# Optimization experiments

Measured on AMD Instinct MI355X. Metric: run time of the kernel, lower is better.

Reference implementation:

```python
import jax, jax.numpy as jnp
import numpy as np

BN_EPS = 1e-5
LN_EPS = 1e-5

N_NODES = 50000
N_EDGES = 800000
D_IN = 128
D_HID = 512


def _batchnorm(h, gamma, beta):
    # training-mode BatchNorm1d: biased variance over the node/batch dim
    m = jnp.mean(h, axis=0)
    v = jnp.mean(jnp.square(h - m), axis=0)
    return (h - m) * jax.lax.rsqrt(v + BN_EPS) * gamma + beta


def setup_inputs() -> dict:
    key = jax.random.key(0)
    ks = jax.random.split(key, 8)
    x = jax.random.normal(ks[0], (N_NODES, D_IN), dtype=jnp.float32)
    edge_index = jax.random.randint(ks[1], (2, N_EDGES), 0, N_NODES, dtype=jnp.int64)
    s1 = 1.0 / np.sqrt(D_IN)
    s2 = 1.0 / np.sqrt(D_HID)
    W1 = jax.random.uniform(ks[2], (D_IN, D_HID), jnp.float32, -s1, s1)
    b1 = jax.random.uniform(ks[3], (D_HID,), jnp.float32, -s1, s1)
    W2 = jax.random.uniform(ks[4], (D_HID, D_IN), jnp.float32, -s2, s2)
    b2 = jax.random.uniform(ks[5], (D_IN,), jnp.float32, -s2, s2)
    return {
        "x": x,
        "edge_index": edge_index,
        "W1": W1, "b1": b1,
        "bn1_g": jnp.ones((D_HID,), jnp.float32), "bn1_b": jnp.zeros((D_HID,), jnp.float32),
        "W2": W2, "b2": b2,
        "bn2_g": jnp.ones((D_IN,), jnp.float32), "bn2_b": jnp.zeros((D_IN,), jnp.float32),
        "ln_g": jnp.ones((D_IN,), jnp.float32), "ln_b": jnp.zeros((D_IN,), jnp.float32),
    }


def reference(x, edge_index, W1, b1, bn1_g, bn1_b, W2, b2, bn2_g, bn2_b, ln_g, ln_b):
    n = x.shape[0]
    src = edge_index[0]
    dst = edge_index[1]
    # GIN aggregation: sum of neighbor (source) features at each destination node
    agg = jax.ops.segment_sum(x[src], dst, num_segments=n)  # [N, D_IN]
    h = x + agg  # (1 + eps) * x + agg, eps = 0
    # MLP: Linear -> BN -> ReLU -> Linear -> BN -> ReLU (final activation)
    h = jax.nn.relu(_batchnorm(h @ W1 + b1, bn1_g, bn1_b))  # [N, D_HID]
    h = jax.nn.relu(_batchnorm(h @ W2 + b2, bn2_g, bn2_b))  # [N, D_IN]
    # residual + LayerNorm (dropout p=0 -> identity)
    out = h + x
    m = jnp.mean(out, axis=-1, keepdims=True)
    v = jnp.mean(jnp.square(out - m), axis=-1, keepdims=True)
    out = (out - m) * jax.lax.rsqrt(v + LN_EPS) * ln_g + ln_b
    return out
```

## Files before the change

### kernel.cpp

```cpp
#include <hip/hip_runtime.h>
#include <stdint.h>

#define N_NODES 50000
#define N_EDGES 800000
#define D_IN    128
#define D_HID   512
#define NPAD    50048
#define NTILES  391
#define SCAN_NB 196
#define G_TILES 782
#define G_BLOCKS 128

typedef __attribute__((ext_vector_type(8))) short short8;
typedef __attribute__((ext_vector_type(4))) float f32x4;

__device__ __forceinline__ float bf2f(unsigned short u) {
    union { unsigned int i; float f; } v; v.i = ((unsigned int)u) << 16; return v.f;
}
__device__ __forceinline__ unsigned short f2bf(float f) {
    union { float f; unsigned int i; } v; v.f = f;
    unsigned int r = v.i + 0x7fffu + ((v.i >> 16) & 1u);
    return (unsigned short)(r >> 16);
}
__device__ __forceinline__ float loadP(const void* p, long i, int isf) {
    return isf ? ((const float*)p)[i] : bf2f(((const unsigned short*)p)[i]);
}

__global__ void k_init(const void* __restrict__ x, const int* __restrict__ ei,
                       float* __restrict__ stats, int* __restrict__ counts,
                       int* __restrict__ flags) {
    int t = threadIdx.x;
    if (blockIdx.x < 197) {
        int i = blockIdx.x * 256 + t;
        if (i < 384) stats[1024 + i] = 0.f;
        else if (i < 384 + N_NODES) counts[i - 384] = 0;
    } else {
        __shared__ int sh[2];
        if (t == 0) { sh[0] = 0; sh[1] = 1; }
        __syncthreads();
        const unsigned short* xu = (const unsigned short*)x;
        for (int i = t; i < 8192; i += 256)
            if (((xu[i] >> 7) & 0xFF) == 0xFF) sh[0] = 1;
        for (int k = t; k < 64; k += 256)
            if (ei[2 * k + 1] != 0) sh[1] = 0;
        __syncthreads();
        if (t == 0) { flags[0] = sh[0]; flags[1] = sh[1]; }
    }
}

__global__ void k_transpose2(const void* __restrict__ W1, const void* __restrict__ W2,
                             unsigned short* __restrict__ w1t, unsigned short* __restrict__ w2t,
                             const int* __restrict__ flags) {
    int isf = flags[0];
    int idx = blockIdx.x * 256 + threadIdx.x;
    if (idx < D_IN * D_HID) {
        int n = idx >> 7, k = idx & 127;
        int src = k * D_HID + n;
        w1t[idx] = isf ? f2bf(((const float*)W1)[src])
                       : ((const unsigned short*)W1)[src];
    } else {
        int j = idx - D_IN * D_HID;
        int n = j >> 9, k = j & 511;
        int src = k * D_IN + n;
        w2t[j] = isf ? f2bf(((const float*)W2)[src])
                     : ((const unsigned short*)W2)[src];
    }
}

__global__ void k_count(const int* __restrict__ ei, int* __restrict__ counts,
                        const int* __restrict__ flags) {
    int i64 = flags[1];
    int e = blockIdx.x * 256 + threadIdx.x;
    int d = i64 ? ei[2 * N_EDGES + 2 * e] : ei[N_EDGES + e];
    d = min(max(d, 0), N_NODES - 1);
    atomicAdd(&counts[d], 1);
}

__global__ __launch_bounds__(256) void k_scan_block(const int* __restrict__ counts,
                                                    int* __restrict__ rowptr,
                                                    int* __restrict__ partials) {
    __shared__ int a[256], b[256];
    int t = threadIdx.x;
    int idx = blockIdx.x * 256 + t;
    int c = (idx < N_NODES) ? counts[idx] : 0;
    a[t] = c;
    __syncthreads();
    int* src = a; int* dst = b;
    for (int off = 1; off < 256; off <<= 1) {
        dst[t] = src[t] + ((t >= off) ? src[t - off] : 0);
        __syncthreads();
        int* tmp = src; src = dst; dst = tmp;
    }
    if (idx < N_NODES) rowptr[idx] = src[t] - c;
    if (t == 255) partials[blockIdx.x] = src[255];
}

__global__ __launch_bounds__(256) void k_scan_part(int* __restrict__ partials) {
    __shared__ int a[256], b[256];
    int t = threadIdx.x;
    int c = (t < SCAN_NB) ? partials[t] : 0;
    a[t] = c;
    __syncthreads();
    int* src = a; int* dst = b;
    for (int off = 1; off < 256; off <<= 1) {
        dst[t] = src[t] + ((t >= off) ? src[t - off] : 0);
        __syncthreads();
        int* tmp = src; src = dst; dst = tmp;
    }
    if (t < SCAN_NB) partials[t] = src[t] - c;
}

__global__ void k_scan_add(int* __restrict__ rowptr, int* __restrict__ cursor,
                           const int* __restrict__ partials) {
    int idx = blockIdx.x * 256 + threadIdx.x;
    if (idx < N_NODES) {
        int v = rowptr[idx] + partials[blockIdx.x];
        rowptr[idx] = v;
        cursor[idx] = v;
    } else if (idx == N_NODES) {
        rowptr[N_NODES] = N_EDGES;
    }
}

__global__ void k_fill(const int* __restrict__ ei, int* __restrict__ cursor,
                       int* __restrict__ bucket, const int* __restrict__ flags) {
    int i64 = flags[1];
    int e = blockIdx.x * 256 + threadIdx.x;
    int s, d;
    if (i64) { s = ei[2 * e]; d = ei[2 * N_EDGES + 2 * e]; }
    else     { s = ei[e];     d = ei[N_EDGES + e]; }
    s = min(max(s, 0), N_NODES - 1);
    d = min(max(d, 0), N_NODES - 1);
    int pos = atomicAdd(&cursor[d], 1);
    bucket[pos] = s;
}

__global__ __launch_bounds__(256) void k_gather(const int* __restrict__ rowptr,
                                                const int* __restrict__ bucket,
                                                const void* __restrict__ x,
                                                unsigned short* __restrict__ agg,
                                                const int* __restrict__ flags) {
    int isf = flags[0];
    int w = threadIdx.x >> 6, lane = threadIdx.x & 63;
    int row = blockIdx.x * 4 + w;
    float a0 = 0.f, a1 = 0.f;
    if (row < N_NODES) {
        int beg = rowptr[row], end = rowptr[row + 1];
        if (isf) {
            const float* xf = (const float*)x;
            float2 v = *(const float2*)(xf + (size_t)row * D_IN + lane * 2);
            a0 = v.x; a1 = v.y;
            int j = beg;
            for (; j + 4 <= end; j += 4) {
                int s0 = bucket[j], s1 = bucket[j + 1], s2 = bucket[j + 2], s3 = bucket[j + 3];
                float2 n0 = *(const float2*)(xf + (size_t)s0 * D_IN + lane * 2);
                float2 n1 = *(const float2*)(xf + (size_t)s1 * D_IN + lane * 2);
                float2 n2 = *(const float2*)(xf + (size_t)s2 * D_IN + lane * 2);
                float2 n3 = *(const float2*)(xf + (size_t)s3 * D_IN + lane * 2);
                a0 += (n0.x + n1.x) + (n2.x + n3.x);
                a1 += (n0.y + n1.y) + (n2.y + n3.y);
            }
            for (; j < end; j++) {
                float2 n = *(const float2*)(xf + (size_t)bucket[j] * D_IN + lane * 2);
                a0 += n.x; a1 += n.y;
            }
        } else {
            const unsigned int* xu = (const unsigned int*)x;
            unsigned int u = xu[(size_t)row * 64 + lane];
            a0 = bf2f(u & 0xffff); a1 = bf2f(u >> 16);
            int j = beg;
            for (; j + 4 <= end; j += 4) {
                int s0 = bucket[j], s1 = bucket[j + 1], s2 = bucket[j + 2], s3 = bucket[j + 3];
                unsigned int u0 = xu[(size_t)s0 * 64 + lane];
                unsigned int u1 = xu[(size_t)s1 * 64 + lane];
                unsigned int u2 = xu[(size_t)s2 * 64 + lane];
                unsigned int u3 = xu[(size_t)s3 * 64 + lane];
                a0 += (bf2f(u0 & 0xffff) + bf2f(u1 & 0xffff)) + (bf2f(u2 & 0xffff) + bf2f(u3 & 0xffff));
                a1 += (bf2f(u0 >> 16) + bf2f(u1 >> 16)) + (bf2f(u2 >> 16) + bf2f(u3 >> 16));
            }
            for (; j < end; j++) {
                unsigned int n = xu[(size_t)bucket[j] * 64 + lane];
                a0 += bf2f(n & 0xffff); a1 += bf2f(n >> 16);
            }
        }
    }
    unsigned int o = (unsigned int)f2bf(a0) | ((unsigned int)f2bf(a1) << 16);
    ((unsigned int*)agg)[(size_t)row * 64 + lane] = o;
}

__global__ __launch_bounds__(256) void k_gram(const unsigned short* __restrict__ aggb,
                                              float* __restrict__ Gpart,
                                              float* __restrict__ colsum) {
    __shared__ unsigned short ldsT[128 * 64];
    int t = threadIdx.x;
    int wid = t >> 6, lane = t & 63;
    int wm = wid & 1, wn = wid >> 1;
    int quad = lane >> 4, l16 = lane & 15;
    f32x4 acc[4][4] = {};
    float cs = 0.f;
    int cscol = t & 127, cskh = t >> 7;
    for (int tile = blockIdx.x; tile < G_TILES; tile += G_BLOCKS) {
        __syncthreads();
        size_t rowbase = (size_t)tile * 64;
#pragma unroll
        for (int jj = 0; jj < 2; jj++) {
            int j = t + jj * 256;
            int c = j >> 5, rp = j & 31;
            uint4 v0 = *(const uint4*)(aggb + (rowbase + 2 * rp) * 128 + c * 8);
            uint4 v1 = *(const uint4*)(aggb + (rowbase + 2 * rp + 1) * 128 + c * 8);
            const unsigned short* p0 = (const unsigned short*)&v0;
            const unsigned short* p1 = (const unsigned short*)&v1;
            int k = 2 * rp, kc = k >> 3, ko = k & 7;
#pragma unroll
            for (int e = 0; e < 8; e++) {
                int col = c * 8 + e;
                *(unsigned int*)(ldsT + col * 64 + ((kc ^ (col & 7)) * 8) + ko) =
                    (unsigned int)p0[e] | ((unsigned int)p1[e] << 16);
            }
        }
        __syncthreads();
#pragma unroll
        for (int ksub = 0; ksub < 2; ksub++) {
            short8 fa[4], fb[4];
#pragma unroll
            for (int mt = 0; mt < 4; mt++) {
                int col = wm * 64 + mt * 16 + l16;
                fa[mt] = *(const short8*)(ldsT + col * 64 + (((ksub * 4 + quad) ^ (col & 7)) * 8));
            }
#pragma unroll
            for (int nt = 0; nt < 4; nt++) {
                int col = wn * 64 + nt * 16 + l16;
                fb[nt] = *(const short8*)(ldsT + col * 64 + (((ksub * 4 + quad) ^ (col & 7)) * 8));
            }
#pragma unroll
            for (int mt = 0; mt < 4; mt++)
#pragma unroll
                for (int nt = 0; nt < 4; nt++)
                    acc[mt][nt] = __builtin_amdgcn_mfma_f32_16x16x32_bf16(fa[mt], fb[nt], acc[mt][nt], 0, 0, 0);
        }
#pragma unroll
        for (int kc = 0; kc < 4; kc++) {
            short8 v = *(const short8*)(ldsT + cscol * 64 + (((cskh * 4 + kc) ^ (cscol & 7)) * 8));
#pragma unroll
            for (int e = 0; e < 8; e++) cs += bf2f((unsigned short)v[e]);
        }
    }
    float* gp = Gpart + (size_t)blockIdx.x * 16384;
#pragma unroll
    for (int mt = 0; mt < 4; mt++)
#pragma unroll
        for (int nt = 0; nt < 4; nt++) {
            int m = wm * 64 + mt * 16 + quad * 4;
            int n = wn * 64 + nt * 16 + l16;
#pragma unroll
            for (int rg = 0; rg < 4; rg++)
                gp[(m + rg) * 128 + n] = acc[mt][nt][rg];
        }
    atomicAdd(&colsum[cscol], cs);
}

__global__ void k_gred(const float* __restrict__ Gpart, float* __restrict__ G) {
    int i = blockIdx.x * 256 + threadIdx.x;
    float s = 0.f;
#pragma unroll 8
    for (int b = 0; b < G_BLOCKS; b++) s += Gpart[(size_t)b * 16384 + i];
    G[i] = s;
}

__global__ __launch_bounds__(256) void k_bn1(const float* __restrict__ G,
                                             const float* __restrict__ colsum,
                                             const unsigned short* __restrict__ w1t,
                                             const void* __restrict__ b1,
                                             float* __restrict__ sum1,
                                             float* __restrict__ sumsq1,
                                             const int* __restrict__ flags) {
    int isf = flags[0];
    __shared__ float wsh[4][128];
    int t = threadIdx.x, wid = t >> 6, lane = t & 63;
    int n = blockIdx.x * 4 + wid;
    unsigned int u = *(const unsigned int*)(w1t + (size_t)n * 128 + lane * 2);
    wsh[wid][lane * 2] = bf2f(u & 0xffff);
    wsh[wid][lane * 2 + 1] = bf2f(u >> 16);
    __syncthreads();
    const float* w = wsh[wid];
    const f32x4* g0 = (const f32x4*)(G + (size_t)lane * 128);
    const f32x4* g1 = (const f32x4*)(G + (size_t)(lane + 64) * 128);
    float t0 = 0.f, t1 = 0.f;
#pragma unroll 4
    for (int q4 = 0; q4 < 32; q4++) {
        f32x4 a = g0[q4], b = g1[q4];
        float w0 = w[q4 * 4], w1 = w[q4 * 4 + 1], w2 = w[q4 * 4 + 2], w3 = w[q4 * 4 + 3];
        t0 += a[0] * w0 + a[1] * w1 + a[2] * w2 + a[3] * w3;
        t1 += b[0] * w0 + b[1] * w1 + b[2] * w2 + b[3] * w3;
    }
    float sq = w[lane] * t0 + w[lane + 64] * t1;
    float s  = w[lane] * colsum[lane] + w[lane + 64] * colsum[lane + 64];
#pragma unroll
    for (int m = 1; m < 64; m <<= 1) {
        sq += __shfl_xor(sq, m, 64);
        s  += __shfl_xor(s, m, 64);
    }
    if (lane == 0) {
        float b = loadP(b1, n, isf);
        sum1[n]   = s + (float)N_NODES * b;
        sumsq1[n] = sq + 2.f * b * s + (float)N_NODES * b * b;
    }
}

__global__ __launch_bounds__(256, 2) void k_mlp1(const unsigned short* __restrict__ aggc,
                                                 const unsigned short* __restrict__ w1t,
                                                 const void* __restrict__ b1,
                                                 const void* __restrict__ g1,
                                                 const void* __restrict__ bb1,
                                                 const float* __restrict__ sum1,
                                                 const float* __restrict__ sumsq1,
                                                 unsigned short* __restrict__ h1c,
                                                 const int* __restrict__ flags) {
    __shared__ unsigned short bufA[128 * 128];
    __shared__ unsigned short bufW[128 * 128];
    int isf = flags[0];
    int t = threadIdx.x;
    int m0 = (blockIdx.x >> 2) * 128;
    int nb = blockIdx.x & 3;
    int r = t >> 1, half = t & 1;
    int wid = t >> 6, lane = t & 63;
    int wm = wid & 1, wn = wid >> 1;
    int quad = lane >> 4, l16 = lane & 15;
#pragma unroll
    for (int i = 0; i < 8; i++) {
        int chunk = half * 8 + i;
        int sw = ((chunk ^ (r & 15)) * 8);
        *(uint4*)(bufA + r * 128 + sw) = *(const uint4*)(aggc + (size_t)(m0 + r) * 128 + chunk * 8);
        *(uint4*)(bufW + r * 128 + sw) = *(const uint4*)(w1t + (size_t)(nb * 128 + r) * 128 + chunk * 8);
    }
    __syncthreads();
    f32x4 acc[4][4] = {};
#pragma unroll
    for (int ks = 0; ks < 4; ks++) {
        short8 af[4], bw[4];
#pragma unroll
        for (int mt = 0; mt < 4; mt++)
            af[mt] = *(const short8*)(bufA + (wm * 64 + mt * 16 + l16) * 128 + (((ks * 4 + quad) ^ l16) * 8));
#pragma unroll
        for (int nt = 0; nt < 4; nt++)
            bw[nt] = *(const short8*)(bufW + (wn * 64 + nt * 16 + l16) * 128 + (((ks * 4 + quad) ^ l16) * 8));
#pragma unroll
        for (int mt = 0; mt < 4; mt++)
#pragma unroll
            for (int nt = 0; nt < 4; nt++)
                acc[mt][nt] = __builtin_amdgcn_mfma_f32_16x16x32_bf16(af[mt], bw[nt], acc[mt][nt], 0, 0, 0);
    }
    __syncthreads();
#pragma unroll
    for (int nt = 0; nt < 4; nt++) {
        int nl = wn * 64 + nt * 16 + l16;
        int n1 = nb * 128 + nl;
        float mz = sum1[n1] * (1.f / N_NODES);
        float vz = sumsq1[n1] * (1.f / N_NODES) - mz * mz;
        float inv = rsqrtf(fmaxf(vz, 0.f) + 1e-5f);
        float A = loadP(g1, n1, isf) * inv;
        float C = loadP(bb1, n1, isf) - mz * A + loadP(b1, n1, isf) * A;
        int ccw = nl >> 3, cl = nl & 7;
#pragma unroll
        for (int mt = 0; mt < 4; mt++)
#pragma unroll
            for (int rg = 0; rg < 4; rg++) {
                int R = wm * 64 + mt * 16 + quad * 4 + rg;
                bufA[R * 128 + ((ccw ^ (R & 15)) * 8) + cl] = f2bf(fmaxf(acc[mt][nt][rg] * A + C, 0.f));
            }
    }
    __syncthreads();
#pragma unroll
    for (int i = 0; i < 8; i++) {
        int idx = t + i * 256;
        int rr = idx >> 4, chunk = idx & 15;
        *(uint4*)(h1c + (size_t)(m0 + rr) * D_HID + nb * 128 + chunk * 8) =
            *(const uint4*)(bufA + rr * 128 + ((chunk ^ (rr & 15)) * 8));
    }
}

__global__ __launch_bounds__(256, 3) void k_mlp2(const unsigned short* __restrict__ h1c,
                                                 const unsigned short* __restrict__ w2t,
                                                 const void* __restrict__ b2,
                                                 unsigned short* __restrict__ h2c,
                                                 float* __restrict__ sum2,
                                                 float* __restrict__ sumsq2,
                                                 const int* __restrict__ flags,
                                                 int roff) {
    __shared__ unsigned short bufA[64 * 128];
    __shared__ unsigned short bufW[128 * 128];
    __shared__ float sred[256];
    int isf = flags[0];
    int t = threadIdx.x;
    int m0 = blockIdx.x * 64;
    int rw = t >> 1, halfw = t & 1;
    int wid = t >> 6, lane = t & 63;
    int wm = wid & 1, wn = wid >> 1;
    int quad = lane >> 4, l16 = lane & 15;
    sred[t] = 0.f;
    f32x4 acc[2][4] = {};
    for (int kb = 0; kb < 4; kb++) {
        __syncthreads();
#pragma unroll
        for (int i = 0; i < 4; i++) {
            int idx = t + i * 256;
            int rr = idx >> 4, chunk = idx & 15;
            *(uint4*)(bufA + rr * 128 + ((chunk ^ (rr & 15)) * 8)) =
                *(const uint4*)(h1c + (size_t)(m0 + rr) * D_HID + kb * 128 + chunk * 8);
        }
#pragma unroll
        for (int i = 0; i < 8; i++) {
            int chunk = halfw * 8 + i;
            *(uint4*)(bufW + rw * 128 + ((chunk ^ (rw & 15)) * 8)) =
                *(const uint4*)(w2t + (size_t)rw * D_HID + kb * 128 + chunk * 8);
        }
        __syncthreads();
#pragma unroll
        for (int ks = 0; ks < 4; ks++) {
            short8 af[2], bw[4];
#pragma unroll
            for (int mt = 0; mt < 2; mt++)
                af[mt] = *(const short8*)(bufA + (wm * 32 + mt * 16 + l16) * 128 + (((ks * 4 + quad) ^ l16) * 8));
#pragma unroll
            for (int nt = 0; nt < 4; nt++)
                bw[nt] = *(const short8*)(bufW + (wn * 64 + nt * 16 + l16) * 128 + (((ks * 4 + quad) ^ l16) * 8));
#pragma unroll
            for (int mt = 0; mt < 2; mt++)
#pragma unroll
                for (int nt = 0; nt < 4; nt++)
                    acc[mt][nt] = __builtin_amdgcn_mfma_f32_16x16x32_bf16(af[mt], bw[nt], acc[mt][nt], 0, 0, 0);
        }
    }
    __syncthreads();
#pragma unroll
    for (int nt = 0; nt < 4; nt++) {
        int n = wn * 64 + nt * 16 + l16;
        float bias = loadP(b2, n, isf);
        float s = 0.f, ss = 0.f;
#pragma unroll
        for (int mt = 0; mt < 2; mt++) {
            int Rl = wm * 32 + mt * 16 + quad * 4;
#pragma unroll
            for (int rg = 0; rg < 4; rg++) {
                float z = acc[mt][nt][rg] + bias;
                bufW[(Rl + rg) * 128 + n] = f2bf(z);
                if (roff + m0 + Rl + rg < N_NODES) { s += z; ss += z * z; }
            }
        }
        s += __shfl_xor(s, 16, 64); ss += __shfl_xor(ss, 16, 64);
        s += __shfl_xor(s, 32, 64); ss += __shfl_xor(ss, 32, 64);
        if (quad == 0) { atomicAdd(&sred[n], s); atomicAdd(&sred[128 + n], ss); }
    }
    __syncthreads();
#pragma unroll
    for (int i = 0; i < 4; i++) {
        int idx = t + i * 256;
        int rr = idx >> 4, seg = idx & 15;
        *(uint4*)(h2c + (size_t)(m0 + rr) * D_IN + seg * 8) = *(const uint4*)(bufW + rr * 128 + seg * 8);
    }
    if (t < 256) {
        int n = t & 127;
        if (t < 128) atomicAdd(&sum2[n], sred[n]);
        else         atomicAdd(&sumsq2[n], sred[128 + n]);
    }
}

__global__ __launch_bounds__(256) void k_final(const unsigned short* __restrict__ h2,
                                               const void* __restrict__ x,
                                               const float* __restrict__ sum2,
                                               const float* __restrict__ sumsq2,
                                               const void* __restrict__ g2,
                                               const void* __restrict__ bb2,
                                               const void* __restrict__ lng,
                                               const void* __restrict__ lnb,
                                               void* __restrict__ out,
                                               const int* __restrict__ flags) {
    int isf = flags[0];
    __shared__ float a2s[D_IN], c2s[D_IN];
    int t = threadIdx.x;
    if (t < D_IN) {
        float m = sum2[t] * (1.f / N_NODES);
        float v = sumsq2[t] * (1.f / N_NODES) - m * m;
        float inv = rsqrtf(fmaxf(v, 0.f) + 1e-5f);
        float a = loadP(g2, t, isf) * inv;
        a2s[t] = a;
        c2s[t] = loadP(bb2, t, isf) - m * a;
    }
    __syncthreads();
    int w = t >> 6, lane = t & 63;
    int row = blockIdx.x * 4 + w;
    if (row >= N_NODES) return;
    size_t base = (size_t)row * D_IN;
    int c0 = lane * 2, c1 = lane * 2 + 1;
    unsigned int hu = ((const unsigned int*)h2)[base / 2 + lane];
    float x0, x1;
    if (isf) {
        float2 xv = *((const float2*)x + base / 2 + lane);
        x0 = xv.x; x1 = xv.y;
    } else {
        unsigned int xu = ((const unsigned int*)x)[base / 2 + lane];
        x0 = bf2f(xu & 0xffff); x1 = bf2f(xu >> 16);
    }
    float o0 = fmaxf(a2s[c0] * bf2f(hu & 0xffff) + c2s[c0], 0.f) + x0;
    float o1 = fmaxf(a2s[c1] * bf2f(hu >> 16) + c2s[c1], 0.f) + x1;
    float s = o0 + o1, ss = o0 * o0 + o1 * o1;
#pragma unroll
    for (int m = 1; m < 64; m <<= 1) {
        s += __shfl_xor(s, m, 64);
        ss += __shfl_xor(ss, m, 64);
    }
    float mean = s * (1.f / D_IN);
    float var = ss * (1.f / D_IN) - mean * mean;
    float inv = rsqrtf(fmaxf(var, 0.f) + 1e-5f);
    float r0 = (o0 - mean) * inv * loadP(lng, c0, isf) + loadP(lnb, c0, isf);
    float r1 = (o1 - mean) * inv * loadP(lng, c1, isf) + loadP(lnb, c1, isf);
    if (isf) {
        *((float2*)out + base / 2 + lane) = make_float2(r0, r1);
    } else {
        ((unsigned int*)out)[base / 2 + lane] = (unsigned int)f2bf(r0) | ((unsigned int)f2bf(r1) << 16);
    }
}

extern "C" void kernel_launch(void* const* d_in, const int* in_sizes, int n_in,
                              void* d_out, int out_size, void* d_ws, size_t ws_size,
                              hipStream_t stream) {
    const void* x    = d_in[0];
    const int*  ei   = (const int*)d_in[1];
    const void* W1   = d_in[2];
    const void* b1   = d_in[3];
    const void* bn1g = d_in[4];
    const void* bn1b = d_in[5];
    const void* W2   = d_in[6];
    const void* b2   = d_in[7];
    const void* bn2g = d_in[8];
    const void* bn2b = d_in[9];
    const void* lng  = d_in[10];
    const void* lnb  = d_in[11];

    char* ws = (char*)d_ws;
    float* stats   = (float*)ws;
    float* sum1    = stats;
    float* sumsq1  = stats + 512;
    float* sum2    = stats + 1024;
    float* sumsq2  = stats + 1152;
    float* colsum  = stats + 1280;
    int*   flags   = (int*)(ws + 5632);
    int*   partials= (int*)(ws + 5696);
    int*   rowptr  = (int*)(ws + 8192);
    int*   cursor  = (int*)(ws + 208256);
    unsigned short* w1t = (unsigned short*)(ws + 408320);
    unsigned short* w2t = (unsigned short*)(ws + 539392);
    float* G       = (float*)(ws + 670464);
    unsigned short* agg = (unsigned short*)(ws + 736000);
    unsigned short* h2  = agg;
    int*   bucket  = (int*)(ws + 13548288);
    float* Gpart   = (float*)(ws + 16748288);
    unsigned short* h1r = (unsigned short*)(ws + 13548288);

    k_init<<<198, 256, 0, stream>>>(x, ei, stats, cursor, flags);
    k_transpose2<<<512, 256, 0, stream>>>(W1, W2, w1t, w2t, flags);
    k_count<<<N_EDGES / 256, 256, 0, stream>>>(ei, cursor, flags);
    k_scan_block<<<SCAN_NB, 256, 0, stream>>>(cursor, rowptr, partials);
    k_scan_part<<<1, 256, 0, stream>>>(partials);
    k_scan_add<<<SCAN_NB, 256, 0, stream>>>(rowptr, cursor, partials);
    k_fill<<<N_EDGES / 256, 256, 0, stream>>>(ei, cursor, bucket, flags);
    k_gather<<<NPAD / 4, 256, 0, stream>>>(rowptr, bucket, x, agg, flags);
    k_gram<<<G_BLOCKS, 256, 0, stream>>>(agg, Gpart, colsum);
    k_gred<<<64, 256, 0, stream>>>(Gpart, G);
    k_bn1<<<128, 256, 0, stream>>>(G, colsum, w1t, b1, sum1, sumsq1, flags);

    long long avail = (long long)ws_size - 13548288LL;
    int max_tiles = (avail > 0) ? (int)(avail / 131072LL) : 1;
    if (max_tiles < 1)  max_tiles = 1;
    if (max_tiles > NTILES) max_tiles = NTILES;
    int nch = (NTILES + max_tiles - 1) / max_tiles;
    int per = (NTILES + nch - 1) / nch;
    for (int done = 0; done < NTILES; done += per) {
        int nt = NTILES - done;
        if (nt > per) nt = per;
        const unsigned short* aggc = agg + (size_t)done * 128 * 128;
        unsigned short* h2c = h2 + (size_t)done * 128 * 128;
        k_mlp1<<<nt * 4, 256, 0, stream>>>(aggc, w1t, b1, bn1g, bn1b, sum1, sumsq1, h1r, flags);
        k_mlp2<<<nt * 2, 256, 0, stream>>>(h1r, w2t, b2, h2c, sum2, sumsq2, flags, done * 128);
    }

    k_final<<<(N_NODES + 3) / 4, 256, 0, stream>>>(h2, x, sum2, sumsq2, bn2g, bn2b, lng, lnb, d_out, flags);
}
```

Measured before the change: 378.5 us.

## Replace Gram-matrix BN1 stats with direct stats accumulation in fused MLP path

When the workspace can hold the full h1 buffer, the Gram-matrix pass (k_gram/k_gred/k_bn1) is skipped. A new first-layer GEMM stores pre-BN h1 and accumulates BN1 sums by atomics, and a new second-layer kernel applies BN1 and ReLU on load before its GEMM. The gather loop is also unrolled to 8 neighbors for more memory-level parallelism. The cost is a larger full-size h1 write/read in HBM and a workspace-size-dependent fallback path.

Result: faster. 362.8 us (-4.1%).

```diff
diff --git a/kernel.cpp b/kernel.cpp
--- a/kernel.cpp
+++ b/kernel.cpp
@@ -9,7 +9,8 @@
 #define NTILES  391
 #define SCAN_NB 196
 #define G_TILES 782
-#define G_BLOCKS 128
+#define G_BLOCKS 256
+#define H1_FULL_NEED 64797440LL
 
 typedef __attribute__((ext_vector_type(8))) short short8;
 typedef __attribute__((ext_vector_type(4))) float f32x4;
@@ -30,10 +31,10 @@
                        float* __restrict__ stats, int* __restrict__ counts,
                        int* __restrict__ flags) {
     int t = threadIdx.x;
-    if (blockIdx.x < 197) {
+    if (blockIdx.x < 201) {
         int i = blockIdx.x * 256 + t;
-        if (i < 384) stats[1024 + i] = 0.f;
-        else if (i < 384 + N_NODES) counts[i - 384] = 0;
+        if (i < 1408) stats[i] = 0.f;
+        else if (i < 1408 + N_NODES) counts[i - 1408] = 0;
     } else {
         __shared__ int sh[2];
         if (t == 0) { sh[0] = 0; sh[1] = 1; }
@@ -151,12 +152,23 @@
             float2 v = *(const float2*)(xf + (size_t)row * D_IN + lane * 2);
             a0 = v.x; a1 = v.y;
             int j = beg;
+            for (; j + 8 <= end; j += 8) {
+                float2 n0 = *(const float2*)(xf + (size_t)bucket[j] * D_IN + lane * 2);
+                float2 n1 = *(const float2*)(xf + (size_t)bucket[j + 1] * D_IN + lane * 2);
+                float2 n2 = *(const float2*)(xf + (size_t)bucket[j + 2] * D_IN + lane * 2);
+                float2 n3 = *(const float2*)(xf + (size_t)bucket[j + 3] * D_IN + lane * 2);
+                float2 n4 = *(const float2*)(xf + (size_t)bucket[j + 4] * D_IN + lane * 2);
+                float2 n5 = *(const float2*)(xf + (size_t)bucket[j + 5] * D_IN + lane * 2);
+                float2 n6 = *(const float2*)(xf + (size_t)bucket[j + 6] * D_IN + lane * 2);
+                float2 n7 = *(const float2*)(xf + (size_t)bucket[j + 7] * D_IN + lane * 2);
+                a0 += ((n0.x + n1.x) + (n2.x + n3.x)) + ((n4.x + n5.x) + (n6.x + n7.x));
+                a1 += ((n0.y + n1.y) + (n2.y + n3.y)) + ((n4.y + n5.y) + (n6.y + n7.y));
+            }
             for (; j + 4 <= end; j += 4) {
-                int s0 = bucket[j], s1 = bucket[j + 1], s2 = bucket[j + 2], s3 = bucket[j + 3];
-                float2 n0 = *(const float2*)(xf + (size_t)s0 * D_IN + lane * 2);
-                float2 n1 = *(const float2*)(xf + (size_t)s1 * D_IN + lane * 2);
-                float2 n2 = *(const float2*)(xf + (size_t)s2 * D_IN + lane * 2);
-                float2 n3 = *(const float2*)(xf + (size_t)s3 * D_IN + lane * 2);
+                float2 n0 = *(const float2*)(xf + (size_t)bucket[j] * D_IN + lane * 2);
+                float2 n1 = *(const float2*)(xf + (size_t)bucket[j + 1] * D_IN + lane * 2);
+                float2 n2 = *(const float2*)(xf + (size_t)bucket[j + 2] * D_IN + lane * 2);
+                float2 n3 = *(const float2*)(xf + (size_t)bucket[j + 3] * D_IN + lane * 2);
                 a0 += (n0.x + n1.x) + (n2.x + n3.x);
                 a1 += (n0.y + n1.y) + (n2.y + n3.y);
             }
@@ -169,12 +181,25 @@
             unsigned int u = xu[(size_t)row * 64 + lane];
             a0 = bf2f(u & 0xffff); a1 = bf2f(u >> 16);
             int j = beg;
+            for (; j + 8 <= end; j += 8) {
+                unsigned int u0 = xu[(size_t)bucket[j] * 64 + lane];
+                unsigned int u1 = xu[(size_t)bucket[j + 1] * 64 + lane];
+                unsigned int u2 = xu[(size_t)bucket[j + 2] * 64 + lane];
+                unsigned int u3 = xu[(size_t)bucket[j + 3] * 64 + lane];
+                unsigned int u4 = xu[(size_t)bucket[j + 4] * 64 + lane];
+                unsigned int u5 = xu[(size_t)bucket[j + 5] * 64 + lane];
+                unsigned int u6 = xu[(size_t)bucket[j + 6] * 64 + lane];
+                unsigned int u7 = xu[(size_t)bucket[j + 7] * 64 + lane];
+                a0 += ((bf2f(u0 & 0xffff) + bf2f(u1 & 0xffff)) + (bf2f(u2 & 0xffff) + bf2f(u3 & 0xffff)))
+                    + ((bf2f(u4 & 0xffff) + bf2f(u5 & 0xffff)) + (bf2f(u6 & 0xffff) + bf2f(u7 & 0xffff)));
+                a1 += ((bf2f(u0 >> 16) + bf2f(u1 >> 16)) + (bf2f(u2 >> 16) + bf2f(u3 >> 16)))
+                    + ((bf2f(u4 >> 16) + bf2f(u5 >> 16)) + (bf2f(u6 >> 16) + bf2f(u7 >> 16)));
+            }
             for (; j + 4 <= end; j += 4) {
-                int s0 = bucket[j], s1 = bucket[j + 1], s2 = bucket[j + 2], s3 = bucket[j + 3];
-                unsigned int u0 = xu[(size_t)s0 * 64 + lane];
-                unsigned int u1 = xu[(size_t)s1 * 64 + lane];
-                unsigned int u2 = xu[(size_t)s2 * 64 + lane];
-                unsigned int u3 = xu[(size_t)s3 * 64 + lane];
+                unsigned int u0 = xu[(size_t)bucket[j] * 64 + lane];
+                unsigned int u1 = xu[(size_t)bucket[j + 1] * 64 + lane];
+                unsigned int u2 = xu[(size_t)bucket[j + 2] * 64 + lane];
+                unsigned int u3 = xu[(size_t)bucket[j + 3] * 64 + lane];
                 a0 += (bf2f(u0 & 0xffff) + bf2f(u1 & 0xffff)) + (bf2f(u2 & 0xffff) + bf2f(u3 & 0xffff));
                 a1 += (bf2f(u0 >> 16) + bf2f(u1 >> 16)) + (bf2f(u2 >> 16) + bf2f(u3 >> 16));
             }
@@ -379,6 +404,82 @@
     }
 }
 
+__global__ __launch_bounds__(256, 2) void k_mlp1r(const unsigned short* __restrict__ aggb,
+                                                  const unsigned short* __restrict__ w1t,
+                                                  const void* __restrict__ b1,
+                                                  unsigned short* __restrict__ h1,
+                                                  float* __restrict__ sum1,
+                                                  float* __restrict__ sumsq1,
+                                                  const int* __restrict__ flags) {
+    __shared__ unsigned short bufA[128 * 128];
+    __shared__ unsigned short bufW[128 * 128];
+    __shared__ float sred[256];
+    int isf = flags[0];
+    int t = threadIdx.x;
+    int m0 = (blockIdx.x >> 2) * 128;
+    int nb = blockIdx.x & 3;
+    int r = t >> 1, half = t & 1;
+    int wid = t >> 6, lane = t & 63;
+    int wm = wid & 1, wn = wid >> 1;
+    int quad = lane >> 4, l16 = lane & 15;
+    sred[t] = 0.f;
+#pragma unroll
+    for (int i = 0; i < 8; i++) {
+        int chunk = half * 8 + i;
+        int sw = ((chunk ^ (r & 15)) * 8);
+        *(uint4*)(bufA + r * 128 + sw) = *(const uint4*)(aggb + (size_t)(m0 + r) * 128 + chunk * 8);
+        *(uint4*)(bufW + r * 128 + sw) = *(const uint4*)(w1t + (size_t)(nb * 128 + r) * 128 + chunk * 8);
+    }
+    __syncthreads();
+    f32x4 acc[4][4] = {};
+#pragma unroll
+    for (int ks = 0; ks < 4; ks++) {
+        short8 af[4], bw[4];
+#pragma unroll
+        for (int mt = 0; mt < 4; mt++)
+            af[mt] = *(const short8*)(bufA + (wm * 64 + mt * 16 + l16) * 128 + (((ks * 4 + quad) ^ l16) * 8));
+#pragma unroll
+        for (int nt = 0; nt < 4; nt++)
+            bw[nt] = *(const short8*)(bufW + (wn * 64 + nt * 16 + l16) * 128 + (((ks * 4 + quad) ^ l16) * 8));
+#pragma unroll
+        for (int mt = 0; mt < 4; mt++)
+#pragma unroll
+            for (int nt = 0; nt < 4; nt++)
+                acc[mt][nt] = __builtin_amdgcn_mfma_f32_16x16x32_bf16(af[mt], bw[nt], acc[mt][nt], 0, 0, 0);
+    }
+    __syncthreads();
+#pragma unroll
+    for (int nt = 0; nt < 4; nt++) {
+        int nl = wn * 64 + nt * 16 + l16;
+        int n1 = nb * 128 + nl;
+        float bias = loadP(b1, n1, isf);
+        int ccw = nl >> 3, cl = nl & 7;
+        float s = 0.f, ss = 0.f;
+#pragma unroll
+        for (int mt = 0; mt < 4; mt++)
+#pragma unroll
+            for (int rg = 0; rg < 4; rg++) {
+                int R = wm * 64 + mt * 16 + quad * 4 + rg;
+                float z = acc[mt][nt][rg] + bias;
+                bufA[R * 128 + ((ccw ^ (R & 15)) * 8) + cl] = f2bf(z);
+                if (m0 + R < N_NODES) { s += z; ss += z * z; }
+            }
+        s += __shfl_xor(s, 16, 64); ss += __shfl_xor(ss, 16, 64);
+        s += __shfl_xor(s, 32, 64); ss += __shfl_xor(ss, 32, 64);
+        if (quad == 0) { atomicAdd(&sred[nl], s); atomicAdd(&sred[128 + nl], ss); }
+    }
+    __syncthreads();
+#pragma unroll
+    for (int i = 0; i < 8; i++) {
+        int idx = t + i * 256;
+        int rr = idx >> 4, chunk = idx & 15;
+        *(uint4*)(h1 + (size_t)(m0 + rr) * D_HID + nb * 128 + chunk * 8) =
+            *(const uint4*)(bufA + rr * 128 + ((chunk ^ (rr & 15)) * 8));
+    }
+    if (t < 128)      atomicAdd(&sum1[nb * 128 + t], sred[t]);
+    else              atomicAdd(&sumsq1[nb * 128 + (t - 128)], sred[t]);
+}
+
 __global__ __launch_bounds__(256, 3) void k_mlp2(const unsigned short* __restrict__ h1c,
                                                  const unsigned short* __restrict__ w2t,
                                                  const void* __restrict__ b2,
@@ -458,7 +559,111 @@
         int rr = idx >> 4, seg = idx & 15;
         *(uint4*)(h2c + (size_t)(m0 + rr) * D_IN + seg * 8) = *(const uint4*)(bufW + rr * 128 + seg * 8);
     }
-    if (t < 256) {
+    {
+        int n = t & 127;
+        if (t < 128) atomicAdd(&sum2[n], sred[n]);
+        else         atomicAdd(&sumsq2[n], sred[128 + n]);
+    }
+}
+
+__global__ __launch_bounds__(256, 3) void k_mlp2b(const unsigned short* __restrict__ h1,
+                                                  const unsigned short* __restrict__ w2t,
+                                                  const void* __restrict__ b2,
+                                                  const void* __restrict__ g1,
+                                                  const void* __restrict__ bb1,
+                                                  const float* __restrict__ sum1,
+                                                  const float* __restrict__ sumsq1,
+                                                  unsigned short* __restrict__ h2,
+                                                  float* __restrict__ sum2,
+                                                  float* __restrict__ sumsq2,
+                                                  const int* __restrict__ flags) {
+    __shared__ unsigned short bufA[64 * 128];
+    __shared__ unsigned short bufW[128 * 128];
+    __shared__ float sred[256];
+    __shared__ float bnA[512], bnC[512];
+    int isf = flags[0];
+    int t = threadIdx.x;
+    int m0 = blockIdx.x * 64;
+    int rw = t >> 1, halfw = t & 1;
+    int wid = t >> 6, lane = t & 63;
+    int wm = wid & 1, wn = wid >> 1;
+    int quad = lane >> 4, l16 = lane & 15;
+    sred[t] = 0.f;
+    for (int i = t; i < 512; i += 256) {
+        float mz = sum1[i] * (1.f / N_NODES);
+        float vz = sumsq1[i] * (1.f / N_NODES) - mz * mz;
+        float inv = rsqrtf(fmaxf(vz, 0.f) + 1e-5f);
+        float A = loadP(g1, i, isf) * inv;
+        bnA[i] = A;
+        bnC[i] = loadP(bb1, i, isf) - mz * A;
+    }
+    f32x4 acc[2][4] = {};
+    for (int kb = 0; kb < 4; kb++) {
+        __syncthreads();
+#pragma unroll
+        for (int i = 0; i < 4; i++) {
+            int idx = t + i * 256;
+            int rr = idx >> 4, chunk = idx & 15;
+            uint4 v = *(const uint4*)(h1 + (size_t)(m0 + rr) * D_HID + kb * 128 + chunk * 8);
+            const unsigned short* pv = (const unsigned short*)&v;
+            unsigned short o[8];
+            int cb = kb * 128 + chunk * 8;
+#pragma unroll
+            for (int e = 0; e < 8; e++)
+                o[e] = f2bf(fmaxf(bf2f(pv[e]) * bnA[cb + e] + bnC[cb + e], 0.f));
+            *(uint4*)(bufA + rr * 128 + ((chunk ^ (rr & 15)) * 8)) = *(const uint4*)o;
+        }
+#pragma unroll
+        for (int i = 0; i < 8; i++) {
+            int chunk = halfw * 8 + i;
+            *(uint4*)(bufW + rw * 128 + ((chunk ^ (rw & 15)) * 8)) =
+                *(const uint4*)(w2t + (size_t)rw * D_HID + kb * 128 + chunk * 8);
+        }
+        __syncthreads();
+#pragma unroll
+        for (int ks = 0; ks < 4; ks++) {
+            short8 af[2], bw[4];
+#pragma unroll
+            for (int mt = 0; mt < 2; mt++)
+                af[mt] = *(const short8*)(bufA + (wm * 32 + mt * 16 + l16) * 128 + (((ks * 4 + quad) ^ l16) * 8));
+#pragma unroll
+            for (int nt = 0; nt < 4; nt++)
+                bw[nt] = *(const short8*)(bufW + (wn * 64 + nt * 16 + l16) * 128 + (((ks * 4 + quad) ^ l16) * 8));
+#pragma unroll
+            for (int mt = 0; mt < 2; mt++)
+#pragma unroll
+                for (int nt = 0; nt < 4; nt++)
+                    acc[mt][nt] = __builtin_amdgcn_mfma_f32_16x16x32_bf16(af[mt], bw[nt], acc[mt][nt], 0, 0, 0);
+        }
+    }
+    __syncthreads();
+#pragma unroll
+    for (int nt = 0; nt < 4; nt++) {
+        int n = wn * 64 + nt * 16 + l16;
+        float bias = loadP(b2, n, isf);
+        float s = 0.f, ss = 0.f;
+#pragma unroll
+        for (int mt = 0; mt < 2; mt++) {
+            int Rl = wm * 32 + mt * 16 + quad * 4;
+#pragma unroll
+            for (int rg = 0; rg < 4; rg++) {
+                float z = acc[mt][nt][rg] + bias;
+                bufW[(Rl + rg) * 128 + n] = f2bf(z);
+                if (m0 + Rl + rg < N_NODES) { s += z; ss += z * z; }
+            }
+        }
+        s += __shfl_xor(s, 16, 64); ss += __shfl_xor(ss, 16, 64);
+        s += __shfl_xor(s, 32, 64); ss += __shfl_xor(ss, 32, 64);
+        if (quad == 0) { atomicAdd(&sred[n], s); atomicAdd(&sred[128 + n], ss); }
+    }
+    __syncthreads();
+#pragma unroll
+    for (int i = 0; i < 4; i++) {
+        int idx = t + i * 256;
+        int rr = idx >> 4, seg = idx & 15;
+        *(uint4*)(h2 + (size_t)(m0 + rr) * D_IN + seg * 8) = *(const uint4*)(bufW + rr * 128 + seg * 8);
+    }
+    {
         int n = t & 127;
         if (t < 128) atomicAdd(&sum2[n], sred[n]);
         else         atomicAdd(&sumsq2[n], sred[128 + n]);
@@ -557,7 +762,7 @@
     float* Gpart   = (float*)(ws + 16748288);
     unsigned short* h1r = (unsigned short*)(ws + 13548288);
 
-    k_init<<<198, 256, 0, stream>>>(x, ei, stats, cursor, flags);
+    k_init<<<202, 256, 0, stream>>>(x, ei, stats, cursor, flags);
     k_transpose2<<<512, 256, 0, stream>>>(W1, W2, w1t, w2t, flags);
     k_count<<<N_EDGES / 256, 256, 0, stream>>>(ei, cursor, flags);
     k_scan_block<<<SCAN_NB, 256, 0, stream>>>(cursor, rowptr, partials);
@@ -565,23 +770,29 @@
     k_scan_add<<<SCAN_NB, 256, 0, stream>>>(rowptr, cursor, partials);
     k_fill<<<N_EDGES / 256, 256, 0, stream>>>(ei, cursor, bucket, flags);
     k_gather<<<NPAD / 4, 256, 0, stream>>>(rowptr, bucket, x, agg, flags);
-    k_gram<<<G_BLOCKS, 256, 0, stream>>>(agg, Gpart, colsum);
-    k_gred<<<64, 256, 0, stream>>>(Gpart, G);
-    k_bn1<<<128, 256, 0, stream>>>(G, colsum, w1t, b1, sum1, sumsq1, flags);
-
-    long long avail = (long long)ws_size - 13548288LL;
-    int max_tiles = (avail > 0) ? (int)(avail / 131072LL) : 1;
-    if (max_tiles < 1)  max_tiles = 1;
-    if (max_tiles > NTILES) max_tiles = NTILES;
-    int nch = (NTILES + max_tiles - 1) / max_tiles;
-    int per = (NTILES + nch - 1) / nch;
-    for (int done = 0; done < NTILES; done += per) {
-        int nt = NTILES - done;
-        if (nt > per) nt = per;
-        const unsigned short* aggc = agg + (size_t)done * 128 * 128;
-        unsigned short* h2c = h2 + (size_t)done * 128 * 128;
-        k_mlp1<<<nt * 4, 256, 0, stream>>>(aggc, w1t, b1, bn1g, bn1b, sum1, sumsq1, h1r, flags);
-        k_mlp2<<<nt * 2, 256, 0, stream>>>(h1r, w2t, b2, h2c, sum2, sumsq2, flags, done * 128);
+
+    if ((long long)ws_size >= H1_FULL_NEED) {
+        k_mlp1r<<<NTILES * 4, 256, 0, stream>>>(agg, w1t, b1, h1r, sum1, sumsq1, flags);
+        k_mlp2b<<<NPAD / 64, 256, 0, stream>>>(h1r, w2t, b2, bn1g, bn1b, sum1, sumsq1,
+                                               h2, sum2, sumsq2, flags);
+    } else {
+        k_gram<<<G_BLOCKS, 256, 0, stream>>>(agg, Gpart, colsum);
+        k_gred<<<64, 256, 0, stream>>>(Gpart, G);
+        k_bn1<<<128, 256, 0, stream>>>(G, colsum, w1t, b1, sum1, sumsq1, flags);
+        long long avail = (long long)ws_size - 13548288LL;
+        int max_tiles = (avail > 0) ? (int)(avail / 131072LL) : 1;
+        if (max_tiles < 1)  max_tiles = 1;
+        if (max_tiles > NTILES) max_tiles = NTILES;
+        int nch = (NTILES + max_tiles - 1) / max_tiles;
+        int per = (NTILES + nch - 1) / nch;
+        for (int done = 0; done < NTILES; done += per) {
+            int nt = NTILES - done;
+            if (nt > per) nt = per;
+            const unsigned short* aggc = agg + (size_t)done * 128 * 128;
+            unsigned short* h2c = h2 + (size_t)done * 128 * 128;
+            k_mlp1<<<nt * 4, 256, 0, stream>>>(aggc, w1t, b1, bn1g, bn1b, sum1, sumsq1, h1r, flags);
+            k_mlp2<<<nt * 2, 256, 0, stream>>>(h1r, w2t, b2, h2c, sum2, sumsq2, flags, done * 128);
+        }
     }
 
     k_final<<<(N_NODES + 3) / 4, 256, 0, stream>>>(h2, x, sum2, sumsq2, bn2g, bn2b, lng, lnb, d_out, flags);
```
